# Optimization experiments

Hardware: AMD Instinct MI355X
Metric: run time of the kernel (lower is better)

## Reference

```python
import jax, jax.numpy as jnp
import numpy as np

NH, DH, BS, HS = 8, 16, 8, 3           # heads, head dim, block size, halo size
WIN = BS + 2 * HS                      # 14
DIM, DIM_V = 256, 256
SCALE = DH ** -0.5


def setup_inputs() -> dict:
    key = jax.random.key(0)
    k1, k2, k3, k4, k5 = jax.random.split(key, 5)
    x = jax.random.normal(k1, (8, DIM, 64, 64), jnp.float32)
    q_w = jax.random.normal(k2, (NH * DH, DIM), jnp.float32) * (DIM ** -0.5)
    kv_w = jax.random.normal(k3, (NH * DH + DIM_V, DIM), jnp.float32) * (DIM ** -0.5)
    height_rel = jax.random.normal(k4, (2 * WIN - 1, DH), jnp.float32) * SCALE
    width_rel = jax.random.normal(k5, (2 * WIN - 1, DH), jnp.float32) * SCALE
    return {"x": x, "q_w": q_w, "kv_w": kv_w, "height_rel": height_rel, "width_rel": width_rel}


def _rel_logits_1d(q, rel_k, perm):
    N, Hq, Wq, d = q.shape
    rel_size = rel_k.shape[0]
    win = (rel_size + 1) // 2
    x = jnp.einsum('nhwd,rd->nhwr', q, rel_k).reshape(N * Hq, Wq, rel_size)
    x = jnp.pad(x, ((0, 0), (0, 0), (0, 1))).reshape(N * Hq, Wq * (rel_size + 1))
    x = jnp.pad(x, ((0, 0), (0, rel_size - Wq))).reshape(N * Hq, Wq + 1, rel_size)
    x = x[:, :Wq, win - 1:]
    x = jnp.broadcast_to(x.reshape(N, Hq, 1, Wq, win), (N, Hq, win, Wq, win))
    return x.transpose(perm)


def _pos_embed(q, height_rel, width_rel):
    Bh, nb, HW, dh = q.shape
    qb = q.reshape(-1, BS, BS, dh)
    rw = _rel_logits_1d(qb, width_rel, (0, 1, 3, 2, 4))
    rh = _rel_logits_1d(qb.transpose(0, 2, 1, 3), height_rel, (0, 3, 1, 4, 2))
    return (rh + rw).reshape(Bh, nb, HW, -1)


def reference(x, q_w, kv_w, height_rel, width_rel):
    B, C, H, W = x.shape
    nHb, nWb = H // BS, W // BS
    nb = nHb * nWb
    dvh = DIM_V // NH

    # q: 1x1 conv + block-unfold -> (B*nh, nb, bs*bs, dh)
    q = jnp.einsum('bchw,oc->bohw', x, q_w)
    q = q.reshape(B, NH, DH, nHb, BS, nWb, BS).transpose(0, 1, 3, 5, 4, 6, 2)
    q = q.reshape(B * NH, nb, BS * BS, DH)

    kv = jnp.einsum('bchw,oc->bohw', x, kv_w)
    kvp = jnp.pad(kv, ((0, 0), (0, 0), (HS, HS), (HS, HS)))
    rows = jnp.arange(nHb)[:, None] * BS + jnp.arange(WIN)[None, :]
    cols = jnp.arange(nWb)[:, None] * BS + jnp.arange(WIN)[None, :]
    wins = kvp[:, :, rows][:, :, :, :, cols]
    wins = wins.transpose(0, 1, 2, 4, 3, 5)
    wins = wins.reshape(B, NH, DH + dvh, nb, WIN * WIN).transpose(0, 1, 3, 4, 2)
    wins = wins.reshape(B * NH, nb, WIN * WIN, DH + dvh)
    k, v = wins[..., :DH], wins[..., DH:]

    attn = jnp.einsum('znqd,znkd->znqk', q, k) * SCALE + _pos_embed(q, height_rel, width_rel)
    attn = jax.nn.softmax(attn, axis=-1)
    out = jnp.einsum('znqk,znkd->znqd', attn, v)        # (B*nh, nb, bs*bs, dvh)

    # fold blocks back to (B, dim_v, H, W)
    out = out.reshape(B, NH, nHb, nWb, BS, BS, dvh).transpose(0, 1, 6, 2, 4, 3, 5)
    return out.reshape(B, DIM_V, H, W)
```

## Files before the change

kernel.cpp:

```cpp
#include <hip/hip_runtime.h>
#include <hip/hip_bf16.h>

#define LOG2E 1.4426950408889634f

typedef __attribute__((ext_vector_type(8))) short bf16x8;
typedef __attribute__((ext_vector_type(4))) float f32x4;
typedef __attribute__((ext_vector_type(16))) float f32x16;

__device__ __forceinline__ short f2bf(float a) {
  __hip_bfloat16 h = __float2bfloat16(a);
  return *reinterpret_cast<short*>(&h);
}
__device__ __forceinline__ unsigned pkbf(float a, float b) {
  return (unsigned)(unsigned short)f2bf(a) | ((unsigned)(unsigned short)f2bf(b) << 16);
}
__device__ __forceinline__ unsigned cvtpk(float a, float b) {
  unsigned r;
  asm("v_cvt_pk_bf16_f32 %0, %1, %2" : "=v"(r) : "v"(a), "v"(b));
  return r;
}
__device__ __forceinline__ float bfu2f(unsigned u16v) {
  unsigned v = u16v << 16; float f; __builtin_memcpy(&f, &v, 4); return f;
}
union FragU8 { unsigned d[4]; bf16x8 v; };
union KU { uint4 u; bf16x8 v; };

__global__ __launch_bounds__(256) void haloattn_zero_border(
    unsigned short* __restrict__ vpln)
{
  unsigned short* pl = vpln + (size_t)blockIdx.x * 5040;
  for (int e = threadIdx.x; e < 944; e += 256) {
    int off;
    if (e < 216) {
      off = e;
    } else if (e < 432) {
      off = 4824 + (e - 216);
    } else {
      const int t = e - 432;
      const int y = 3 + (t >> 3);
      const int cidx = t & 7;
      off = y * 72 + (cidx < 3 ? cidx : cidx + 64);
    }
    pl[off] = 0;
  }
}

__global__ __launch_bounds__(256) void haloattn_cvt(
    const float* __restrict__ x, const float* __restrict__ q_w,
    const float* __restrict__ kv_w, unsigned short* __restrict__ xT,
    unsigned short* __restrict__ w_bf)
{
  __shared__ float Ld[64][68];
  const int t = threadIdx.x;
  const int pt = blockIdx.x, kt = blockIdx.y, b = blockIdx.z;
  {
    const int flat = ((b << 2) + kt) * 64 + pt;
    const int idx = flat * 64 + (t & 63);
    if (t < 64) {
      const float wv = (idx < 32768) ? q_w[idx] : kv_w[idx - 32768];
      w_bf[idx] = (unsigned short)f2bf(wv);
    }
  }
  const float* xb = x + ((size_t)b * 256 + (kt << 6)) * 4096 + (pt << 6);
#pragma unroll
  for (int ps = 0; ps < 4; ++ps) {
    const int kloc = (ps << 4) + (t >> 4);
    const int ploc = (t & 15) << 2;
    float4 v = *(const float4*)(xb + (size_t)kloc * 4096 + ploc);
    *(float4*)&Ld[kloc][ploc] = v;
  }
  __syncthreads();
  const int pl = t >> 2;
  const int ks = (t & 3) << 4;
  float f[16];
#pragma unroll
  for (int i = 0; i < 16; ++i) f[i] = Ld[ks + i][pl];
  uint4 o0, o1;
  o0.x = pkbf(f[0], f[1]);   o0.y = pkbf(f[2], f[3]);
  o0.z = pkbf(f[4], f[5]);   o0.w = pkbf(f[6], f[7]);
  o1.x = pkbf(f[8], f[9]);   o1.y = pkbf(f[10], f[11]);
  o1.z = pkbf(f[12], f[13]); o1.w = pkbf(f[14], f[15]);
  unsigned short* op = xT + ((size_t)(b << 12) + (pt << 6) + pl) * 256 + (kt << 6) + ks;
  *(uint4*)op = o0;
  *(uint4*)(op + 8) = o1;
}

__global__ __launch_bounds__(512, 4) void haloattn_proj_mfma(
    const unsigned short* __restrict__ xT, const unsigned short* __restrict__ w_bf,
    unsigned short* __restrict__ q_bf, unsigned short* __restrict__ kbuf,
    unsigned short* __restrict__ vpln)
{
  __shared__ unsigned short Wt[256][68];
  __shared__ unsigned short Xt[128][68];
  const int tid = threadIdx.x;
  const int w = tid >> 6, l = tid & 63;
  const int b = blockIdx.z, oBase = blockIdx.y << 8, pBase = blockIdx.x << 7;
  const int wm = w >> 1, wn = w & 1;
  const int g = l >> 4, c = l & 15;

  f32x4 acc[4][4] = {};

  const int srow = tid >> 3;
  const int se3  = (tid & 7) << 3;

  for (int chk = 0; chk < 4; ++chk) {
    const int k0 = chk << 6;
#pragma unroll
    for (int ps = 0; ps < 4; ++ps) {
      const int row = (ps << 6) + srow;
      uint4 wv = *(const uint4*)(w_bf + (size_t)(oBase + row) * 256 + k0 + se3);
      char* dst = (char*)&Wt[0][0] + row * 136 + (se3 << 1);
      *(uint2*)dst = make_uint2(wv.x, wv.y);
      *(uint2*)(dst + 8) = make_uint2(wv.z, wv.w);
    }
#pragma unroll
    for (int ps = 0; ps < 2; ++ps) {
      const int p = (ps << 6) + srow;
      uint4 xv = *(const uint4*)(xT + ((size_t)(b << 12) + pBase + p) * 256 + k0 + se3);
      char* dst = (char*)&Xt[0][0] + p * 136 + (se3 << 1);
      *(uint2*)dst = make_uint2(xv.x, xv.y);
      *(uint2*)(dst + 8) = make_uint2(xv.z, xv.w);
    }
    __syncthreads();
#pragma unroll
    for (int kk = 0; kk < 2; ++kk) {
      FragU8 bfr[4];
#pragma unroll
      for (int nf = 0; nf < 4; ++nf) {
        const char* src = (const char*)&Xt[0][0]
            + ((wn << 6) + (nf << 4) + c) * 136 + (kk << 6) + (g << 4);
        uint2 lo = *(const uint2*)src, hi2 = *(const uint2*)(src + 8);
        bfr[nf].d[0] = lo.x; bfr[nf].d[1] = lo.y;
        bfr[nf].d[2] = hi2.x; bfr[nf].d[3] = hi2.y;
      }
#pragma unroll
      for (int mf = 0; mf < 4; ++mf) {
        const char* src = (const char*)&Wt[0][0]
            + ((wm << 6) + (mf << 4) + c) * 136 + (kk << 6) + (g << 4);
        uint2 lo = *(const uint2*)src, hi2 = *(const uint2*)(src + 8);
        FragU8 af;
        af.d[0] = lo.x; af.d[1] = lo.y; af.d[2] = hi2.x; af.d[3] = hi2.y;
#pragma unroll
        for (int nf = 0; nf < 4; ++nf)
          acc[mf][nf] = __builtin_amdgcn_mfma_f32_16x16x32_bf16(af.v, bfr[nf].v, acc[mf][nf], 0, 0, 0);
      }
    }
    __syncthreads();
  }
#pragma unroll
  for (int mf = 0; mf < 4; ++mf) {
    const int o = oBase + (wm << 6) + (mf << 4) + (g << 2);
#pragma unroll
    for (int nf = 0; nf < 4; ++nf) {
      const int p = pBase + (wn << 6) + (nf << 4) + c;
      if (o < 128) {
        uint2 pk2 = make_uint2(pkbf(acc[mf][nf][0], acc[mf][nf][1]),
                               pkbf(acc[mf][nf][2], acc[mf][nf][3]));
        const int head = o >> 4;
        const int z = (b << 3) + head;
        const int y = p >> 6, xx = p & 63;
        const int nbb = ((y >> 3) << 3) + (xx >> 3);
        const int qi = ((y & 7) << 3) + (xx & 7);
        *(uint2*)(q_bf + (((size_t)z * 64 + nbb) * 64 + qi) * 16 + (o & 15)) = pk2;
      } else {
        const int ch = o - 128;
        const int head = (ch * 1366) >> 16;
        const int wi = ch - head * 48;
        const int b8h = (b << 3) + head;
        if (wi < 16) {
          uint2 pk2 = make_uint2(pkbf(acc[mf][nf][0], acc[mf][nf][1]),
                                 pkbf(acc[mf][nf][2], acc[mf][nf][3]));
          *(uint2*)(kbuf + ((size_t)b8h * 4096 + p) * 16 + wi) = pk2;
        } else {
          const int d = wi - 16;
          const int y = p >> 6, xx = p & 63;
          unsigned short* vp = vpln + (size_t)(b8h * 32 + d) * 5040
                               + (size_t)(y + 3) * 72 + (xx + 3);
          vp[0]     = (unsigned short)f2bf(acc[mf][nf][0]);
          vp[5040]  = (unsigned short)f2bf(acc[mf][nf][1]);
          vp[10080] = (unsigned short)f2bf(acc[mf][nf][2]);
          vp[15120] = (unsigned short)f2bf(acc[mf][nf][3]);
        }
      }
    }
  }
}

__global__ __launch_bounds__(64, 2) void haloattn_attn_direct(
    const unsigned short* __restrict__ q_bf, const unsigned short* __restrict__ kbuf,
    const unsigned short* __restrict__ vpln,
    const float* __restrict__ height_rel, const float* __restrict__ width_rel,
    float* __restrict__ out)
{
  __shared__ __align__(16) unsigned short SM[5376];

  const int l = threadIdx.x;
  const int q32 = l & 31, hi = l >> 5;
  const int wg = blockIdx.x;
  const int swz = ((wg & 7) << 9) | (wg >> 3);
  const int z = swz >> 6;
  const int nb = swz & 63;
  const int b = z >> 3, head = z & 7;
  const int bi = nb >> 3, bj = nb & 7;
  const int swapA = (l ^ 32) << 2;
  const f32x16 z16 = {};
  const float qs = 0.25f * LOG2E;

  const unsigned short* qtile = q_bf + ((size_t)z * 64 + nb) * 1024;
  bf16x8 qfrag[2];
  qfrag[0] = *(const bf16x8*)(qtile + q32 * 16 + 8 * hi);
  qfrag[1] = *(const bf16x8*)(qtile + (32 + q32) * 16 + 8 * hi);

  unsigned short* HRs = SM;
  unsigned short* WRs = SM + 768;
  if (l < 54) {
    const int u = l >> 1, d0 = (l & 1) << 3;
    float4 a = *(const float4*)(height_rel + u * 16 + d0);
    float4 b4 = *(const float4*)(height_rel + u * 16 + d0 + 4);
    uint4 o;
    o.x = cvtpk(a.x * LOG2E, a.y * LOG2E);
    o.y = cvtpk(a.z * LOG2E, a.w * LOG2E);
    o.z = cvtpk(b4.x * LOG2E, b4.y * LOG2E);
    o.w = cvtpk(b4.z * LOG2E, b4.w * LOG2E);
    *(uint4*)(HRs + u * 24 + d0) = o;
    a = *(const float4*)(width_rel + u * 16 + d0);
    b4 = *(const float4*)(width_rel + u * 16 + d0 + 4);
    o.x = cvtpk(a.x * LOG2E, a.y * LOG2E);
    o.y = cvtpk(a.z * LOG2E, a.w * LOG2E);
    o.z = cvtpk(b4.x * LOG2E, b4.y * LOG2E);
    o.w = cvtpk(b4.z * LOG2E, b4.w * LOG2E);
    *(uint4*)(WRs + u * 24 + d0) = o;
  } else {
    const int t = l - 54;
    const int u = 27 + (t >> 1), d0 = (t & 1) << 3;
    uint4 o = {};
    *(uint4*)(HRs + u * 24 + d0) = o;
    *(uint4*)(WRs + u * 24 + d0) = o;
  }
  __syncthreads();

  {
    bf16x8 hfr = *(const bf16x8*)((const char*)HRs + q32 * 48 + 16 * hi);
    bf16x8 wfr = *(const bf16x8*)((const char*)WRs + q32 * 48 + 16 * hi);
    f32x16 h0 = __builtin_amdgcn_mfma_f32_32x32x16_bf16(hfr, qfrag[0], z16, 0, 0, 0);
    f32x16 h1 = __builtin_amdgcn_mfma_f32_32x32x16_bf16(hfr, qfrag[1], z16, 0, 0, 0);
    f32x16 w0 = __builtin_amdgcn_mfma_f32_32x32x16_bf16(wfr, qfrag[0], z16, 0, 0, 0);
    f32x16 w1 = __builtin_amdgcn_mfma_f32_32x32x16_bf16(wfr, qfrag[1], z16, 0, 0, 0);
    __syncthreads();
#pragma unroll
    for (int r = 0; r < 16; ++r) {
      const int u = (r & 3) + 8 * (r >> 2) + 4 * hi;
      if (u >= 6 && u < 27) {
        const int rr = u - 6;
        SM[rr * 64 + q32]               = (unsigned short)f2bf(h0[r]);
        SM[(21 + rr) * 64 + q32]        = (unsigned short)f2bf(h1[r]);
        SM[2688 + rr * 64 + q32]        = (unsigned short)f2bf(w0[r]);
        SM[2688 + (21 + rr) * 64 + q32] = (unsigned short)f2bf(w1[r]);
      }
    }
  }
  __syncthreads();

  const int qw = q32 & 7;
  float wreg[2][8];
#pragma unroll
  for (int nt = 0; nt < 2; ++nt)
#pragma unroll
    for (int t = 0; t < 8; ++t) {
      const int jt = (t < 4 ? t : t + 4) + 4 * hi;
      if (jt < 14)
        wreg[nt][t] = bfu2f(SM[2688 + (nt * 21 + 7 - qw + jt) * 64 + q32]);
      else
        wreg[nt][t] = -1e30f;
    }

  const int qh0 = q32 >> 3;
  const unsigned short* Hp0 = SM + (7 - qh0) * 64 + q32;
  const unsigned short* Hp1 = SM + (24 - qh0) * 64 + q32;

  const int jj = q32 & 15, ir = q32 >> 4;
  const int xx = bj * 8 + jj - 3;
  const bool jok = (jj < 14) && ((unsigned)xx < 64u);
  const unsigned short* kb = kbuf + ((size_t)((b << 3) + head) * 4096 + xx) * 16 + 8 * hi;
  const int yy0 = bi * 8 + ir - 3;
  const unsigned short* vb = vpln + (size_t)(((b << 3) + head) * 32 + q32) * 5040
                             + (bi * 8) * 72 + bj * 8 + 8 * hi;

  f32x16 acc[2] = {};
  float lrow[2] = {0.f, 0.f};

  KU k4; k4.u = make_uint4(0, 0, 0, 0);
  if (jok && (unsigned)yy0 < 64u) k4.u = *(const uint4*)(kb + (size_t)yy0 * 1024);
  bf16x8 v0n = *(const bf16x8*)(vb);
  bf16x8 v1n = *(const bf16x8*)(vb + 72);

  for (int c = 0; c < 7; ++c) {
    const bf16x8 kf = k4.v;
    const bf16x8 vf0 = v0n, vf1 = v1n;
    if (c < 6) {
      const int yy = yy0 + 2 * (c + 1);
      KU kn; kn.u = make_uint4(0, 0, 0, 0);
      if (jok && (unsigned)yy < 64u) kn.u = *(const uint4*)(kb + (size_t)yy * 1024);
      k4 = kn;
      v0n = *(const bf16x8*)(vb + (2 * c + 2) * 72);
      v1n = *(const bf16x8*)(vb + (2 * c + 3) * 72);
    }
#pragma unroll
    for (int nt = 0; nt < 2; ++nt) {
      f32x16 Cs = __builtin_amdgcn_mfma_f32_32x32x16_bf16(kf, qfrag[nt], z16, 0, 0, 0);
      const unsigned short* Hp = nt ? Hp1 : Hp0;
      const float hA = bfu2f(Hp[(2 * c) * 64]);
      const float hB = bfu2f(Hp[(2 * c + 1) * 64]);
      float p[16];
#pragma unroll
      for (int r = 0; r < 16; ++r) {
        const float wv = wreg[nt][(r & 3) + 4 * ((r >> 2) & 1)];
        const float h = (r < 8) ? hA : hB;
        p[r] = exp2f(fmaf(Cs[r], qs, h + wv));
      }
      {
        float s0 = (p[0] + p[1]) + (p[2] + p[3]);
        float s1 = (p[4] + p[5]) + (p[6] + p[7]);
        float s2 = (p[8] + p[9]) + (p[10] + p[11]);
        float s3 = (p[12] + p[13]) + (p[14] + p[15]);
        lrow[nt] += (s0 + s1) + (s2 + s3);
      }
      unsigned dw[8], xw[8];
#pragma unroll
      for (int k = 0; k < 8; ++k) dw[k] = cvtpk(p[2 * k], p[2 * k + 1]);
#pragma unroll
      for (int k = 0; k < 8; ++k)
        xw[k] = (unsigned)__builtin_amdgcn_ds_bpermute(swapA, (int)dw[k]);
      FragU8 f0, f1;
      f0.d[0] = hi ? xw[2] : dw[0];
      f0.d[1] = hi ? xw[3] : dw[1];
      f0.d[2] = hi ? dw[2] : xw[0];
      f0.d[3] = hi ? dw[3] : xw[1];
      f1.d[0] = hi ? xw[6] : dw[4];
      f1.d[1] = hi ? xw[7] : dw[5];
      f1.d[2] = hi ? dw[6] : xw[4];
      f1.d[3] = hi ? dw[7] : xw[5];
      acc[nt] = __builtin_amdgcn_mfma_f32_32x32x16_bf16(vf0, f0.v, acc[nt], 0, 0, 0);
      acc[nt] = __builtin_amdgcn_mfma_f32_32x32x16_bf16(vf1, f1.v, acc[nt], 0, 0, 0);
    }
  }

#pragma unroll
  for (int nt = 0; nt < 2; ++nt) {
    const float L = lrow[nt] + __shfl_xor(lrow[nt], 32);
    const float invL = 1.f / L;
    const int qt = nt * 32 + q32;
    const int yq = bi * 8 + (qt >> 3);
    const int xq = bj * 8 + (q32 & 7);
    float* obase = out + ((size_t)(b * 256 + head * 32) * 4096) + yq * 64 + xq;
#pragma unroll
    for (int r = 0; r < 16; ++r) {
      const int d = (r & 3) + 8 * (r >> 2) + 4 * hi;
      obase[(size_t)d * 4096] = acc[nt][r] * invL;
    }
  }
}

extern "C" void kernel_launch(void* const* d_in, const int* in_sizes, int n_in,
                              void* d_out, int out_size, void* d_ws, size_t ws_size,
                              hipStream_t stream) {
  const float* x          = (const float*)d_in[0];
  const float* q_w        = (const float*)d_in[1];
  const float* kv_w       = (const float*)d_in[2];
  const float* height_rel = (const float*)d_in[3];
  const float* width_rel  = (const float*)d_in[4];
  float* out = (float*)d_out;

  unsigned short* q_bf = (unsigned short*)d_ws;
  unsigned short* xT   = q_bf + (size_t)4194304;
  unsigned short* w_bf = xT + (size_t)8388608;
  unsigned short* kbuf = w_bf + (size_t)131072;
  unsigned short* vpln = kbuf + (size_t)4194304;

  haloattn_zero_border<<<2048, 256, 0, stream>>>(vpln);
  haloattn_cvt<<<dim3(64, 4, 8), 256, 0, stream>>>(x, q_w, kv_w, xT, w_bf);
  haloattn_proj_mfma<<<dim3(32, 2, 8), 512, 0, stream>>>(xT, w_bf, q_bf, kbuf, vpln);
  haloattn_attn_direct<<<4096, 64, 0, stream>>>(q_bf, kbuf, vpln,
                                                height_rel, width_rel, out);
}
```

Before: 71.54 us.

## Split attention key chunks across two waves and fold border zeroing into cvt

The attention kernel now runs two waves per block. Each wave handles a disjoint subset of the seven key-row chunks (4 and 3), and the partial accumulators and row sums are combined through shared memory before normalisation and store. Each wave then writes one query half. This doubles the parallelism per attention tile to shorten the serial chunk loop. The cost is an extra LDS reduction and two barriers. Separately, the vpln border zeroing is merged into the cvt kernel, which removes one launch.

After: 90.09 us. +25.9%, slower.

```diff
diff --git a/kernel.cpp b/kernel.cpp
--- a/kernel.cpp
+++ b/kernel.cpp
@@ -25,40 +25,37 @@
 union FragU8 { unsigned d[4]; bf16x8 v; };
 union KU { uint4 u; bf16x8 v; };
 
-__global__ __launch_bounds__(256) void haloattn_zero_border(
-    unsigned short* __restrict__ vpln)
-{
-  unsigned short* pl = vpln + (size_t)blockIdx.x * 5040;
-  for (int e = threadIdx.x; e < 944; e += 256) {
-    int off;
-    if (e < 216) {
-      off = e;
-    } else if (e < 432) {
-      off = 4824 + (e - 216);
-    } else {
-      const int t = e - 432;
-      const int y = 3 + (t >> 3);
-      const int cidx = t & 7;
-      off = y * 72 + (cidx < 3 ? cidx : cidx + 64);
-    }
-    pl[off] = 0;
-  }
-}
-
 __global__ __launch_bounds__(256) void haloattn_cvt(
     const float* __restrict__ x, const float* __restrict__ q_w,
     const float* __restrict__ kv_w, unsigned short* __restrict__ xT,
-    unsigned short* __restrict__ w_bf)
+    unsigned short* __restrict__ w_bf, unsigned short* __restrict__ vpln)
 {
   __shared__ float Ld[64][68];
   const int t = threadIdx.x;
   const int pt = blockIdx.x, kt = blockIdx.y, b = blockIdx.z;
+  const int flat = ((b << 2) + kt) * 64 + pt;
   {
-    const int flat = ((b << 2) + kt) * 64 + pt;
     const int idx = flat * 64 + (t & 63);
     if (t < 64) {
       const float wv = (idx < 32768) ? q_w[idx] : kv_w[idx - 32768];
       w_bf[idx] = (unsigned short)f2bf(wv);
+    }
+  }
+  {
+    unsigned short* pl = vpln + (size_t)flat * 5040;
+    for (int e = t; e < 944; e += 256) {
+      int off;
+      if (e < 216) {
+        off = e;
+      } else if (e < 432) {
+        off = 4824 + (e - 216);
+      } else {
+        const int tt = e - 432;
+        const int y = 3 + (tt >> 3);
+        const int cidx = tt & 7;
+        off = y * 72 + (cidx < 3 ? cidx : cidx + 64);
+      }
+      pl[off] = 0;
     }
   }
   const float* xb = x + ((size_t)b * 256 + (kt << 6)) * 4096 + (pt << 6);
@@ -186,7 +183,7 @@
   }
 }
 
-__global__ __launch_bounds__(64, 2) void haloattn_attn_direct(
+__global__ __launch_bounds__(128, 4) void haloattn_attn_direct(
     const unsigned short* __restrict__ q_bf, const unsigned short* __restrict__ kbuf,
     const unsigned short* __restrict__ vpln,
     const float* __restrict__ height_rel, const float* __restrict__ width_rel,
@@ -194,7 +191,9 @@
 {
   __shared__ __align__(16) unsigned short SM[5376];
 
-  const int l = threadIdx.x;
+  const int tid = threadIdx.x;
+  const int w = tid >> 6;
+  const int l = tid & 63;
   const int q32 = l & 31, hi = l >> 5;
   const int wg = blockIdx.x;
   const int swz = ((wg & 7) << 9) | (wg >> 3);
@@ -213,8 +212,8 @@
 
   unsigned short* HRs = SM;
   unsigned short* WRs = SM + 768;
-  if (l < 54) {
-    const int u = l >> 1, d0 = (l & 1) << 3;
+  if (tid < 54) {
+    const int u = tid >> 1, d0 = (tid & 1) << 3;
     float4 a = *(const float4*)(height_rel + u * 16 + d0);
     float4 b4 = *(const float4*)(height_rel + u * 16 + d0 + 4);
     uint4 o;
@@ -230,8 +229,8 @@
     o.z = cvtpk(b4.x * LOG2E, b4.y * LOG2E);
     o.w = cvtpk(b4.z * LOG2E, b4.w * LOG2E);
     *(uint4*)(WRs + u * 24 + d0) = o;
-  } else {
-    const int t = l - 54;
+  } else if (tid < 64) {
+    const int t = tid - 54;
     const int u = 27 + (t >> 1), d0 = (t & 1) << 3;
     uint4 o = {};
     *(uint4*)(HRs + u * 24 + d0) = o;
@@ -247,15 +246,17 @@
     f32x16 w0 = __builtin_amdgcn_mfma_f32_32x32x16_bf16(wfr, qfrag[0], z16, 0, 0, 0);
     f32x16 w1 = __builtin_amdgcn_mfma_f32_32x32x16_bf16(wfr, qfrag[1], z16, 0, 0, 0);
     __syncthreads();
-#pragma unroll
-    for (int r = 0; r < 16; ++r) {
-      const int u = (r & 3) + 8 * (r >> 2) + 4 * hi;
-      if (u >= 6 && u < 27) {
-        const int rr = u - 6;
-        SM[rr * 64 + q32]               = (unsigned short)f2bf(h0[r]);
-        SM[(21 + rr) * 64 + q32]        = (unsigned short)f2bf(h1[r]);
-        SM[2688 + rr * 64 + q32]        = (unsigned short)f2bf(w0[r]);
-        SM[2688 + (21 + rr) * 64 + q32] = (unsigned short)f2bf(w1[r]);
+    if (w == 0) {
+#pragma unroll
+      for (int r = 0; r < 16; ++r) {
+        const int u = (r & 3) + 8 * (r >> 2) + 4 * hi;
+        if (u >= 6 && u < 27) {
+          const int rr = u - 6;
+          SM[rr * 64 + q32]               = (unsigned short)f2bf(h0[r]);
+          SM[(21 + rr) * 64 + q32]        = (unsigned short)f2bf(h1[r]);
+          SM[2688 + rr * 64 + q32]        = (unsigned short)f2bf(w0[r]);
+          SM[2688 + (21 + rr) * 64 + q32] = (unsigned short)f2bf(w1[r]);
+        }
       }
     }
   }
@@ -286,18 +287,25 @@
   const unsigned short* vb = vpln + (size_t)(((b << 3) + head) * 32 + q32) * 5040
                              + (bi * 8) * 72 + bj * 8 + 8 * hi;
 
+  const int c0w = w ? 4 : 0;
+  const int ncw = w ? 3 : 4;
+
   f32x16 acc[2] = {};
   float lrow[2] = {0.f, 0.f};
 
   KU k4; k4.u = make_uint4(0, 0, 0, 0);
-  if (jok && (unsigned)yy0 < 64u) k4.u = *(const uint4*)(kb + (size_t)yy0 * 1024);
-  bf16x8 v0n = *(const bf16x8*)(vb);
-  bf16x8 v1n = *(const bf16x8*)(vb + 72);
-
-  for (int c = 0; c < 7; ++c) {
+  {
+    const int yy = yy0 + 2 * c0w;
+    if (jok && (unsigned)yy < 64u) k4.u = *(const uint4*)(kb + (size_t)yy * 1024);
+  }
+  bf16x8 v0n = *(const bf16x8*)(vb + (2 * c0w) * 72);
+  bf16x8 v1n = *(const bf16x8*)(vb + (2 * c0w + 1) * 72);
+
+  for (int ci = 0; ci < ncw; ++ci) {
+    const int c = c0w + ci;
     const bf16x8 kf = k4.v;
     const bf16x8 vf0 = v0n, vf1 = v1n;
-    if (c < 6) {
+    if (ci < ncw - 1) {
       const int yy = yy0 + 2 * (c + 1);
       KU kn; kn.u = make_uint4(0, 0, 0, 0);
       if (jok && (unsigned)yy < 64u) kn.u = *(const uint4*)(kb + (size_t)yy * 1024);
@@ -345,19 +353,40 @@
     }
   }
 
-#pragma unroll
-  for (int nt = 0; nt < 2; ++nt) {
-    const float L = lrow[nt] + __shfl_xor(lrow[nt], 32);
-    const float invL = 1.f / L;
-    const int qt = nt * 32 + q32;
-    const int yq = bi * 8 + (qt >> 3);
-    const int xq = bj * 8 + (q32 & 7);
-    float* obase = out + ((size_t)(b * 256 + head * 32) * 4096) + yq * 64 + xq;
-#pragma unroll
-    for (int r = 0; r < 16; ++r) {
-      const int d = (r & 3) + 8 * (r >> 2) + 4 * hi;
-      obase[(size_t)d * 4096] = acc[nt][r] * invL;
-    }
+  __syncthreads();
+  float* F = (float*)SM;
+  if (w == 0) {
+#pragma unroll
+    for (int r = 0; r < 16; ++r) F[l * 17 + r] = acc[1][r];
+    F[l * 17 + 16] = lrow[1];
+  } else {
+#pragma unroll
+    for (int r = 0; r < 16; ++r) F[1088 + l * 17 + r] = acc[0][r];
+    F[1088 + l * 17 + 16] = lrow[0];
+  }
+  __syncthreads();
+  const int nt = w;
+  float am[16];
+  float lm;
+  if (w == 0) {
+#pragma unroll
+    for (int r = 0; r < 16; ++r) am[r] = acc[0][r] + F[1088 + l * 17 + r];
+    lm = lrow[0] + F[1088 + l * 17 + 16];
+  } else {
+#pragma unroll
+    for (int r = 0; r < 16; ++r) am[r] = acc[1][r] + F[l * 17 + r];
+    lm = lrow[1] + F[l * 17 + 16];
+  }
+  const float L = lm + __shfl_xor(lm, 32);
+  const float invL = 1.f / L;
+  const int qt = nt * 32 + q32;
+  const int yq = bi * 8 + (qt >> 3);
+  const int xq = bj * 8 + (q32 & 7);
+  float* obase = out + ((size_t)(b * 256 + head * 32) * 4096) + yq * 64 + xq;
+#pragma unroll
+  for (int r = 0; r < 16; ++r) {
+    const int d = (r & 3) + 8 * (r >> 2) + 4 * hi;
+    obase[(size_t)d * 4096] = am[r] * invL;
   }
 }
 
@@ -377,9 +406,8 @@
   unsigned short* kbuf = w_bf + (size_t)131072;
   unsigned short* vpln = kbuf + (size_t)4194304;
 
-  haloattn_zero_border<<<2048, 256, 0, stream>>>(vpln);
-  haloattn_cvt<<<dim3(64, 4, 8), 256, 0, stream>>>(x, q_w, kv_w, xT, w_bf);
+  haloattn_cvt<<<dim3(64, 4, 8), 256, 0, stream>>>(x, q_w, kv_w, xT, w_bf, vpln);
   haloattn_proj_mfma<<<dim3(32, 2, 8), 512, 0, stream>>>(xT, w_bf, q_bf, kbuf, vpln);
-  haloattn_attn_direct<<<4096, 64, 0, stream>>>(q_bf, kbuf, vpln,
-                                                height_rel, width_rel, out);
-}
+  haloattn_attn_direct<<<4096, 128, 0, stream>>>(q_bf, kbuf, vpln,
+                                                 height_rel, width_rel, out);
+}
```
